# Kernel tuning notes

Hardware: AMD Instinct MI355X
Metric: run time of the kernel (lower is better)

## Reference

```python
import jax, jax.numpy as jnp
import numpy as np
import math

SQRT32 = math.sqrt(32.0)


def _l2norm(x, eps=1e-12):
    # matches torch.nn.functional.normalize(dim=-1): x / max(||x||, eps)
    n = jnp.linalg.norm(x, axis=-1, keepdims=True)
    return x / jnp.maximum(n, eps)


def setup_inputs() -> dict:
    key = jax.random.key(0)
    k1, k2 = jax.random.split(key)
    z = jax.random.normal(k1, (8, 256, 32, 32), dtype=jnp.float32)
    # trunc_normal_(std=0.02) init approximated by scaled normal
    embed_weight = jax.random.normal(k2, (16384, 256), dtype=jnp.float32) * 0.02
    return {"z": z, "embed_weight": embed_weight}


def reference(z, embed_weight):
    # z: [b, d, h, w] channel-first -> pack to [b*h*w, d]
    b, d, h, w = z.shape
    zf = jnp.transpose(z, (0, 2, 3, 1)).reshape(-1, d)  # [N, d]

    # l2_norm=True, no predefined codebook: distance = -z @ normalize(E)^T
    ew = _l2norm(embed_weight)                          # [K, d]
    dist = -(zf @ ew.T)                                 # [N, K]
    min_encoding_indices = jnp.argmin(dist, axis=1)     # [N]

    # gather UNnormalized embedding rows, then normalize (as in source)
    z_q = _l2norm(embed_weight[min_encoding_indices])   # [N, d]

    # straight-through estimator
    z_q = zf + jax.lax.stop_gradient(z_q - zf)

    loss = jnp.zeros((1,), dtype=z.dtype)

    # unpack to [b, h, w, d]
    zq_bhwd = z_q.reshape(b, h, w, d)
    # torch .long() truncates toward zero; astype(int) does the same
    bit_indices = (zq_bhwd * SQRT32).astype(jnp.int32) + 4
    zq_out = jnp.transpose(zq_bhwd, (0, 3, 1, 2))       # [b, d, h, w]

    return zq_out, min_encoding_indices, bit_indices, loss
```

## Files before the change

kernel.cpp:

```cpp
#include <hip/hip_runtime.h>
#include <math.h>

#define D      256
#define K      16384
#define NPTS   8192
#define DELTA  0.2f
#define LCAP   512
#define MAXCAP 4000000u

#define O_IDX  2097152
#define O_BIT  2105344
#define O_LOSS 4202496

typedef __attribute__((ext_vector_type(8))) short bf16x8;
typedef __attribute__((ext_vector_type(4))) float f32x4;
typedef unsigned long long u64;

__device__ __forceinline__ unsigned f2s(float f) {
    unsigned u = __float_as_uint(f);
    return (u & 0x80000000u) ? ~u : (u | 0x80000000u);
}
__device__ __forceinline__ float s2f(unsigned s) {
    return __uint_as_float((s & 0x80000000u) ? (s & 0x7fffffffu) : ~s);
}
__device__ __forceinline__ unsigned short f2bf(float f) {
    unsigned u = __float_as_uint(f);
    u += 0x7fffu + ((u >> 16) & 1u);
    return (unsigned short)(u >> 16);
}

__device__ __forceinline__ void gload16(const unsigned short* g, unsigned short* l) {
    __builtin_amdgcn_global_load_lds(
        (const __attribute__((address_space(1))) unsigned int*)g,
        (__attribute__((address_space(3))) unsigned int*)l, 16, 0, 0);
}


__global__ __launch_bounds__(256) void prep(const float* __restrict__ E,
                                            const float* __restrict__ z,
                                            float* __restrict__ den,
                                            unsigned short* __restrict__ ewbT,
                                            unsigned short* __restrict__ zfbT,
                                            float* __restrict__ zf32,
                                            unsigned* __restrict__ gmax,
                                            u64* __restrict__ keys,
                                            unsigned* __restrict__ cnt) {
    const int blk = blockIdx.x, tid = threadIdx.x;
    if (blk < 512) {
        const int lane = tid & 63, wave = tid >> 6;
        if (blk < 32)        gmax[blk * 256 + tid] = 0u;
        else if (blk < 64)   keys[(blk - 32) * 256 + tid] = 0ull;
        else if (blk == 64 && tid < 2) cnt[tid] = 0u;
        #pragma unroll
        for (int j = 0; j < 8; ++j) {
            const int row = blk * 32 + wave * 8 + j;
            const float4 v = *(const float4*)(E + (size_t)row * D + lane * 4);
            float ss = v.x * v.x + v.y * v.y + v.z * v.z + v.w * v.w;
            #pragma unroll
            for (int o = 1; o < 64; o <<= 1) ss += __shfl_xor(ss, o);
            const float dn = fmaxf(sqrtf(ss), 1e-12f);
            const unsigned lo = (unsigned)f2bf(v.x / dn) | ((unsigned)f2bf(v.y / dn) << 16);
            const unsigned hi = (unsigned)f2bf(v.z / dn) | ((unsigned)f2bf(v.w / dn) << 16);
            *(uint2*)(ewbT + ((size_t)(lane >> 1) * K + row) * 8 + (lane & 1) * 4)
                = make_uint2(lo, hi);
            if (lane == 0) den[row] = dn;
        }
    } else {
        const int bi = blk - 512;
        const int b = bi >> 4, hw0 = (bi & 15) * 64;
        __shared__ float t[64][65];
        for (int dc = 0; dc < D; dc += 64) {
            #pragma unroll
            for (int it = 0; it < 16; ++it) {
                const int idx = it * 256 + tid;
                const int dl = idx >> 6, hw = idx & 63;
                t[dl][hw] = z[(size_t)(b * 256 + dc + dl) * 1024 + hw0 + hw];
            }
            __syncthreads();
            #pragma unroll
            for (int it = 0; it < 16; ++it) {
                const int idx = it * 256 + tid;
                const int pl = idx >> 6, dl = idx & 63;
                const float v = t[dl][pl];
                const int p = b * 1024 + hw0 + pl, k = dc + dl;
                zfbT[((size_t)(k >> 3) * NPTS + p) * 8 + (k & 7)] = f2bf(v);
                zf32[(size_t)p * D + k] = v;
            }
            __syncthreads();
        }
    }
}


#define STAGE(buf, t)                                                               \
    do {                                                                            \
        const size_t oA_ = (size_t)(t) * (4 * NPTS * 8);                            \
        const size_t oB_ = (size_t)(t) * (4 * K * 8);                               \
        gload16(gA0_ + oA_, &sA[buf][tid * 8]);                                     \
        gload16(gA1_ + oA_, &sA[buf][2048 + tid * 8]);                              \
        gload16(gB0_ + oB_, &sB[buf][tid * 8]);                                     \
        gload16(gB1_ + oB_, &sB[buf][2048 + tid * 8]);                              \
    } while (0)

#define COMPUTE(buf)                                                                \
    do {                                                                            \
        bf16x8 af_[4], bf_[4];                                                      \
        const unsigned short* a_ = &sA[buf][(size_t)sbA_ * 8];                      \
        const unsigned short* b_ = &sB[buf][(size_t)sbB_ * 8];                      \
        _Pragma("unroll")                                                           \
        for (int mt = 0; mt < 4; ++mt) {                                            \
            af_[mt] = *(const bf16x8*)(a_ + mt * 128);                              \
            bf_[mt] = *(const bf16x8*)(b_ + mt * 128);                              \
        }                                                                           \
        __builtin_amdgcn_s_setprio(1);                                              \
        _Pragma("unroll")                                                           \
        for (int mt = 0; mt < 4; ++mt)                                              \
            _Pragma("unroll")                                                       \
            for (int nt = 0; nt < 4; ++nt)                                          \
                acc[mt][nt] = __builtin_amdgcn_mfma_f32_16x16x32_bf16(af_[mt], bf_[nt], \
                                                                      acc[mt][nt], 0, 0, 0); \
        __builtin_amdgcn_s_setprio(0);                                              \
    } while (0)

#define WAITBAR(VM)                                                                 \
    asm volatile("s_waitcnt vmcnt(" VM ")" ::: "memory");                           \
    __builtin_amdgcn_s_barrier();                                                   \
    asm volatile("" ::: "memory");

#define GEMM_CORE()                                                                 \
    __shared__ unsigned short sA[3][4096];                                          \
    __shared__ unsigned short sB[3][4096];                                          \
    f32x4 acc[4][4];                                                                \
    _Pragma("unroll")                                                               \
    for (int i_ = 0; i_ < 4; ++i_)                                                  \
        _Pragma("unroll")                                                           \
        for (int j_ = 0; j_ < 4; ++j_) acc[i_][j_] = (f32x4){0.f, 0.f, 0.f, 0.f};   \
    const int q0_ = tid >> 7, q1_ = q0_ + 2, pp_ = tid & 127;                       \
    const unsigned short* gA0_ = zfbT + ((size_t)q0_ * NPTS + m0 + (pp_ ^ (q0_ << 1))) * 8; \
    const unsigned short* gA1_ = zfbT + ((size_t)q1_ * NPTS + m0 + (pp_ ^ (q1_ << 1))) * 8; \
    const unsigned short* gB0_ = ewbT + ((size_t)q0_ * K + n0 + (pp_ ^ (q0_ << 1))) * 8; \
    const unsigned short* gB1_ = ewbT + ((size_t)q1_ * K + n0 + (pp_ ^ (q1_ << 1))) * 8; \
    const int sbA_ = quad * 128 + ((wm * 64 + col) ^ (quad << 1));                  \
    const int sbB_ = quad * 128 + ((wn * 64 + col) ^ (quad << 1));                  \
    STAGE(0, 0);                                                                    \
    STAGE(1, 1);                                                                    \
    WAITBAR("4") STAGE(2, 2); COMPUTE(0);                                           \
    WAITBAR("4") STAGE(0, 3); COMPUTE(1);                                           \
    WAITBAR("4") STAGE(1, 4); COMPUTE(2);                                           \
    WAITBAR("4") STAGE(2, 5); COMPUTE(0 + 0);                        \
    WAITBAR("4") STAGE(0, 6); COMPUTE(1);                            \
    WAITBAR("4") STAGE(1, 7); COMPUTE(2);                            \
    WAITBAR("4")              COMPUTE(0);                            \
    WAITBAR("0")              COMPUTE(1);

__global__ __launch_bounds__(256, 3) void score_seed(const unsigned short* __restrict__ zfbT,
                                                     const unsigned short* __restrict__ ewbT,
                                                     unsigned* __restrict__ gmax,
                                                     u64* __restrict__ cand,
                                                     unsigned* __restrict__ cnt,
                                                     unsigned cap) {
    __shared__ unsigned thrS[128];
    __shared__ u64 lbuf[LCAP];
    __shared__ unsigned lcount, lbase;

    const int tid = threadIdx.x, lane = tid & 63, wave = tid >> 6;
    const int quad = lane >> 4, col = lane & 15;
    const int wm = wave >> 1, wn = wave & 1;
    const int m0 = blockIdx.x * 128;
    const int n0 = blockIdx.y * 128;
    const int shsrc = lane & 48;

    if (tid < 128) thrS[tid] = 0u;
    if (tid == 0) lcount = 0u;

    GEMM_CORE()
    __syncthreads();

    float red[4][4];
    #pragma unroll
    for (int mt = 0; mt < 4; ++mt)
        #pragma unroll
        for (int r = 0; r < 4; ++r)
            red[mt][r] = fmaxf(fmaxf(acc[mt][0][r], acc[mt][1][r]),
                               fmaxf(acc[mt][2][r], acc[mt][3][r]));
    #pragma unroll
    for (int off = 1; off < 16; off <<= 1)
        #pragma unroll
        for (int mt = 0; mt < 4; ++mt)
            #pragma unroll
            for (int r = 0; r < 4; ++r)
                red[mt][r] = fmaxf(red[mt][r], __shfl_xor(red[mt][r], off));
    #pragma unroll
    for (int mt = 0; mt < 4; ++mt)
        #pragma unroll
        for (int r = 0; r < 4; ++r) {
            const int pl = wm * 64 + mt * 16 + quad * 4 + r;
            unsigned cur = 0;
            if (col == 0) {
                const unsigned enc = f2s(red[mt][r]);
                const unsigned old = atomicMax(&thrS[pl], enc);
                cur = old > enc ? old : enc;
            }
            cur = (unsigned)__shfl((int)cur, shsrc);
            red[mt][r] = s2f(cur) - DELTA;
        }

    const int ncode0 = n0 + wn * 64 + col;
    #pragma unroll
    for (int mt = 0; mt < 4; ++mt) {
        #pragma unroll
        for (int r = 0; r < 4; ++r) {
            const float tp = red[mt][r];
            const unsigned pt = m0 + wm * 64 + mt * 16 + quad * 4 + r;
            #pragma unroll
            for (int nt = 0; nt < 4; ++nt) {
                const float v = acc[mt][nt][r];
                if (v >= tp) {
                    const unsigned slot = atomicAdd(&lcount, 1u);
                    const u64 e = ((u64)((pt << 14) | (unsigned)(ncode0 + nt * 16)) << 32)
                                  | f2s(v);
                    if (slot < LCAP) lbuf[slot] = e;
                    else {
                        const unsigned g = atomicAdd(cnt, 1u);
                        if (g < cap) cand[g] = e;
                    }
                }
            }
        }
    }

    __syncthreads();
    if (tid < 128) atomicMax(&gmax[m0 + tid], thrS[tid]);
    const unsigned m_ = lcount < LCAP ? lcount : LCAP;
    if (tid == 0) lbase = atomicAdd(cnt, m_);
    __syncthreads();
    for (unsigned i = tid; i < m_; i += 256) {
        const unsigned g = lbase + i;
        if (g < cap) cand[g] = lbuf[i];
    }
}

__global__ __launch_bounds__(256, 3) void score_main(const unsigned short* __restrict__ zfbT,
                                                     const unsigned short* __restrict__ ewbT,
                                                     const unsigned* __restrict__ gmax,
                                                     u64* __restrict__ cand,
                                                     unsigned* __restrict__ cnt,
                                                     unsigned cap) {
    __shared__ float thrL[128];
    __shared__ u64 lbuf[LCAP];
    __shared__ unsigned lcount, lbase;

    const int tid = threadIdx.x, lane = tid & 63, wave = tid >> 6;
    const int quad = lane >> 4, col = lane & 15;
    const int wm = wave >> 1, wn = wave & 1;
    const int m0 = blockIdx.x * 128;
    const int n0 = (16 + blockIdx.y) * 128;

    if (tid < 128) thrL[tid] = s2f(gmax[m0 + tid]) - DELTA;
    if (tid == 0) lcount = 0u;

    GEMM_CORE()
    __syncthreads();

    const int ncode0 = n0 + wn * 64 + col;
    #pragma unroll
    for (int mt = 0; mt < 4; ++mt) {
        #pragma unroll
        for (int r = 0; r < 4; ++r) {
            const int pl = wm * 64 + mt * 16 + quad * 4 + r;
            const float tp = thrL[pl];
            #pragma unroll
            for (int nt = 0; nt < 4; ++nt) {
                const float v = acc[mt][nt][r];
                if (v >= tp) {
                    const unsigned slot = atomicAdd(&lcount, 1u);
                    const u64 e = ((u64)(((unsigned)pl + m0) << 14 | (unsigned)(ncode0 + nt * 16)) << 32)
                                  | f2s(v);
                    if (slot < LCAP) lbuf[slot] = e;
                    else {
                        const unsigned g = atomicAdd(cnt, 1u);
                        if (g < cap) cand[g] = e;
                    }
                }
            }
        }
    }

    __syncthreads();
    const unsigned m_ = lcount < LCAP ? lcount : LCAP;
    if (tid == 0) lbase = atomicAdd(cnt, m_);
    __syncthreads();
    for (unsigned i = tid; i < m_; i += 256) {
        const unsigned g = lbase + i;
        if (g < cap) cand[g] = lbuf[i];
    }
}

__global__ __launch_bounds__(256) void cand_max(const u64* __restrict__ cand,
                                                const unsigned* __restrict__ cnt,
                                                unsigned* __restrict__ gmax,
                                                unsigned cap) {
    const unsigned total = min(cnt[0], cap);
    const unsigned stride = gridDim.x * 256;
    for (unsigned i = blockIdx.x * 256 + threadIdx.x; i < total; i += stride) {
        const u64 e = cand[i];
        atomicMax(&gmax[(unsigned)(e >> 46)], (unsigned)(e & 0xffffffffull));
    }
}

__global__ __launch_bounds__(256) void rescore(const float* __restrict__ zf32,
                                               const float* __restrict__ E,
                                               const float* __restrict__ den,
                                               const unsigned* __restrict__ gmax,
                                               const u64* __restrict__ cand,
                                               const unsigned* __restrict__ cnt,
                                               u64* __restrict__ keys,
                                               unsigned cap) {
    const unsigned total = min(cnt[0], cap);
    const int lane = threadIdx.x & 63;
    const unsigned w = (blockIdx.x * 256 + threadIdx.x) >> 6;
    const unsigned nw = gridDim.x * 4;
    for (unsigned base = w * 64; base < total; base += nw * 64) {
        const unsigned i = base + lane;
        u64 e = 0;
        bool keep = false;
        if (i < total) {
            e = cand[i];
            const int p = (int)(e >> 46);
            keep = (s2f((unsigned)(e & 0xffffffffull)) >= s2f(gmax[p]) - DELTA);
        }
        u64 mask = __ballot(keep);
        while (mask) {
            const int src = __ffsll((long long)mask) - 1;
            mask &= mask - 1;
            const unsigned pc = (unsigned)__shfl((int)(unsigned)(e >> 32), src);
            const int p = pc >> 14, c = pc & 16383;
            const float dinv = 1.0f / den[c];
            const float4 a = *(const float4*)(zf32 + (size_t)p * D + lane * 4);
            const float4 b = *(const float4*)(E + (size_t)c * D + lane * 4);
            float sv = fmaf(a.x, b.x * dinv, fmaf(a.y, b.y * dinv,
                       fmaf(a.z, b.z * dinv, a.w * (b.w * dinv))));
            #pragma unroll
            for (int o = 1; o < 64; o <<= 1) sv += __shfl_xor(sv, o);
            if (lane == 0)
                atomicMax(keys + p, ((u64)f2s(sv) << 32) | (unsigned)(16383 - c));
        }
    }
}

__global__ __launch_bounds__(256) void finalize(const float* __restrict__ E,
                                                const float* __restrict__ den,
                                                const u64* __restrict__ keys,
                                                float* __restrict__ out) {
    __shared__ float t[32][257];
    __shared__ int sIdx[32];
    __shared__ float sDen[32];
    const int tid = threadIdx.x;
    const int n0 = blockIdx.x * 32;
    if (tid < 32) {
        const u64 key = keys[n0 + tid];
        const int idx = 16383 - (int)(unsigned)(key & 0xffffffffull);
        sIdx[tid] = idx;
        sDen[tid] = den[idx];
        out[O_IDX + n0 + tid] = (float)idx;
    }
    __syncthreads();
    const float S = 5.65685424949238019520675489683895f;
    #pragma unroll 4
    for (int i = 0; i < 32; ++i) {
        const float v = E[(size_t)sIdx[i] * D + tid] / sDen[i];
        t[i][tid] = v;
        out[O_BIT + (size_t)(n0 + i) * D + tid] = (float)((int)(v * S) + 4);
    }
    __syncthreads();
    const int b = n0 >> 10, hw0 = n0 & 1023;
    const int hwl = tid & 31, cg = tid >> 5;
    #pragma unroll 4
    for (int cc = 0; cc < 32; ++cc) {
        const int c = cc * 8 + cg;
        out[(size_t)(b * 256 + c) * 1024 + hw0 + hwl] = t[hwl][c];
    }
    if (n0 == 0 && tid == 0) out[O_LOSS] = 0.0f;
}

extern "C" void kernel_launch(void* const* d_in, const int* in_sizes, int n_in,
                              void* d_out, int out_size, void* d_ws, size_t ws_size,
                              hipStream_t stream) {
    const float* z = (const float*)d_in[0];
    const float* E = (const float*)d_in[1];
    float* out = (float*)d_out;

    char* w = (char*)d_ws;
    unsigned short* ewbT = (unsigned short*)w;  w += (size_t)K * D * 2;
    unsigned short* zfbT = (unsigned short*)w;  w += (size_t)NPTS * D * 2;
    float*          zf32 = (float*)w;           w += (size_t)NPTS * D * 4;
    u64*            keys = (u64*)w;             w += (size_t)NPTS * 8;
    float*          den  = (float*)w;           w += (size_t)K * 4;
    unsigned*       gmax = (unsigned*)w;        w += (size_t)NPTS * 4;
    unsigned*       cnt  = (unsigned*)w;        w += 256;
    u64*            cand = (u64*)w;
    const size_t fixed = (size_t)(w - (char*)d_ws);
    const size_t avail = ws_size > fixed ? (ws_size - fixed) / 8 : 0;
    const unsigned cap = (unsigned)(avail < (size_t)MAXCAP ? avail : (size_t)MAXCAP);

    prep<<<640, 256, 0, stream>>>(E, z, den, ewbT, zfbT, zf32, gmax, keys, cnt);

    dim3 gpre(NPTS / 128, 16);
    score_seed<<<gpre, 256, 0, stream>>>(zfbT, ewbT, gmax, cand, cnt, cap);
    dim3 gmain(NPTS / 128, 112);
    score_main<<<gmain, 256, 0, stream>>>(zfbT, ewbT, gmax, cand, cnt, cap);

    cand_max<<<256, 256, 0, stream>>>(cand, cnt, gmax, cap);
    rescore<<<1024, 256, 0, stream>>>(zf32, E, den, gmax, cand, cnt, keys, cap);
    finalize<<<NPTS / 32, 256, 0, stream>>>(E, den, keys, out);
}
```

Before: 260.9 us.

## Enlarge GEMM tiles to 256x256 with 512 threads, double-buffered K64 stages

```diff
diff --git a/kernel.cpp b/kernel.cpp
--- a/kernel.cpp
+++ b/kernel.cpp
@@ -5,7 +5,7 @@
 #define K      16384
 #define NPTS   8192
 #define DELTA  0.2f
-#define LCAP   512
+#define LCAP   2048
 #define MAXCAP 4000000u
 
 #define O_IDX  2097152
@@ -33,6 +33,10 @@
     __builtin_amdgcn_global_load_lds(
         (const __attribute__((address_space(1))) unsigned int*)g,
         (__attribute__((address_space(3))) unsigned int*)l, 16, 0, 0);
+}
+
+__device__ __forceinline__ unsigned lds_off(const void* p) {
+    return (unsigned)(size_t)(const __attribute__((address_space(3))) void*)p;
 }
 
 
@@ -94,27 +98,47 @@
 
 #define STAGE(buf, t)                                                               \
     do {                                                                            \
-        const size_t oA_ = (size_t)(t) * (4 * NPTS * 8);                            \
-        const size_t oB_ = (size_t)(t) * (4 * K * 8);                               \
-        gload16(gA0_ + oA_, &sA[buf][tid * 8]);                                     \
-        gload16(gA1_ + oA_, &sA[buf][2048 + tid * 8]);                              \
-        gload16(gB0_ + oB_, &sB[buf][tid * 8]);                                     \
-        gload16(gB1_ + oB_, &sB[buf][2048 + tid * 8]);                              \
+        const size_t oA_ = (size_t)(t) * (8u * NPTS * 8);                           \
+        const size_t oB_ = (size_t)(t) * (8u * K * 8);                              \
+        unsigned short* dA_ = &sA[buf][0][0][0];                                    \
+        unsigned short* dB_ = &sB[buf][0][0][0];                                    \
+        gload16(gA0_ + oA_, dA_ + (size_t)tid * 8);                                 \
+        gload16(gA1_ + oA_, dA_ + (size_t)(512 + tid) * 8);                         \
+        gload16(gA2_ + oA_, dA_ + (size_t)(1024 + tid) * 8);                        \
+        gload16(gA3_ + oA_, dA_ + (size_t)(1536 + tid) * 8);                        \
+        gload16(gB0_ + oB_, dB_ + (size_t)tid * 8);                                 \
+        gload16(gB1_ + oB_, dB_ + (size_t)(512 + tid) * 8);                         \
+        gload16(gB2_ + oB_, dB_ + (size_t)(1024 + tid) * 8);                        \
+        gload16(gB3_ + oB_, dB_ + (size_t)(1536 + tid) * 8);                        \
     } while (0)
 
-#define COMPUTE(buf)                                                                \
+#define RKK(buf, AA, BB)                                                            \
     do {                                                                            \
-        bf16x8 af_[4], bf_[4];                                                      \
-        const unsigned short* a_ = &sA[buf][(size_t)sbA_ * 8];                      \
-        const unsigned short* b_ = &sB[buf][(size_t)sbB_ * 8];                      \
-        _Pragma("unroll")                                                           \
-        for (int mt = 0; mt < 4; ++mt) {                                            \
-            af_[mt] = *(const bf16x8*)(a_ + mt * 128);                              \
-            bf_[mt] = *(const bf16x8*)(b_ + mt * 128);                              \
-        }                                                                           \
+        const unsigned a__ = (AA) + (unsigned)((buf) * 32768);                      \
+        const unsigned b__ = (BB) + (unsigned)((buf) * 32768);                      \
+        asm volatile("ds_read_b128 %0, %1"             : "=v"(af_[0]) : "v"(a__));  \
+        asm volatile("ds_read_b128 %0, %1 offset:256"  : "=v"(af_[1]) : "v"(a__));  \
+        asm volatile("ds_read_b128 %0, %1 offset:512"  : "=v"(af_[2]) : "v"(a__));  \
+        asm volatile("ds_read_b128 %0, %1 offset:768"  : "=v"(af_[3]) : "v"(a__));  \
+        asm volatile("ds_read_b128 %0, %1 offset:1024" : "=v"(af_[4]) : "v"(a__));  \
+        asm volatile("ds_read_b128 %0, %1 offset:1280" : "=v"(af_[5]) : "v"(a__));  \
+        asm volatile("ds_read_b128 %0, %1 offset:1536" : "=v"(af_[6]) : "v"(a__));  \
+        asm volatile("ds_read_b128 %0, %1 offset:1792" : "=v"(af_[7]) : "v"(a__));  \
+        asm volatile("ds_read_b128 %0, %1"             : "=v"(bf_[0]) : "v"(b__));  \
+        asm volatile("ds_read_b128 %0, %1 offset:256"  : "=v"(bf_[1]) : "v"(b__));  \
+        asm volatile("ds_read_b128 %0, %1 offset:512"  : "=v"(bf_[2]) : "v"(b__));  \
+        asm volatile("ds_read_b128 %0, %1 offset:768"  : "=v"(bf_[3]) : "v"(b__));  \
+    } while (0)
+
+#define LGKM_SB                                                                     \
+    asm volatile("s_waitcnt lgkmcnt(0)" ::: "memory");                              \
+    __builtin_amdgcn_sched_barrier(0);
+
+#define MFMAS                                                                       \
+    do {                                                                            \
         __builtin_amdgcn_s_setprio(1);                                              \
         _Pragma("unroll")                                                           \
-        for (int mt = 0; mt < 4; ++mt)                                              \
+        for (int mt = 0; mt < 8; ++mt)                                              \
             _Pragma("unroll")                                                       \
             for (int nt = 0; nt < 4; ++nt)                                          \
                 acc[mt][nt] = __builtin_amdgcn_mfma_f32_16x16x32_bf16(af_[mt], bf_[nt], \
@@ -127,58 +151,94 @@
     __builtin_amdgcn_s_barrier();                                                   \
     asm volatile("" ::: "memory");
 
+#define BARFENCE                                                                    \
+    __builtin_amdgcn_s_barrier();                                                   \
+    asm volatile("" ::: "memory");
+
 #define GEMM_CORE()                                                                 \
-    __shared__ unsigned short sA[3][4096];                                          \
-    __shared__ unsigned short sB[3][4096];                                          \
-    f32x4 acc[4][4];                                                                \
+    __shared__ unsigned short sA[2][8][256][8];                                     \
+    __shared__ unsigned short sB[2][8][256][8];                                     \
+    f32x4 acc[8][4];                                                                \
     _Pragma("unroll")                                                               \
-    for (int i_ = 0; i_ < 4; ++i_)                                                  \
+    for (int i_ = 0; i_ < 8; ++i_)                                                  \
         _Pragma("unroll")                                                           \
         for (int j_ = 0; j_ < 4; ++j_) acc[i_][j_] = (f32x4){0.f, 0.f, 0.f, 0.f};   \
-    const int q0_ = tid >> 7, q1_ = q0_ + 2, pp_ = tid & 127;                       \
-    const unsigned short* gA0_ = zfbT + ((size_t)q0_ * NPTS + m0 + (pp_ ^ (q0_ << 1))) * 8; \
-    const unsigned short* gA1_ = zfbT + ((size_t)q1_ * NPTS + m0 + (pp_ ^ (q1_ << 1))) * 8; \
-    const unsigned short* gB0_ = ewbT + ((size_t)q0_ * K + n0 + (pp_ ^ (q0_ << 1))) * 8; \
-    const unsigned short* gB1_ = ewbT + ((size_t)q1_ * K + n0 + (pp_ ^ (q1_ << 1))) * 8; \
-    const int sbA_ = quad * 128 + ((wm * 64 + col) ^ (quad << 1));                  \
-    const int sbB_ = quad * 128 + ((wn * 64 + col) ^ (quad << 1));                  \
+    bf16x8 af_[8], bf_[4];                                                          \
+    const int th_ = tid & 255, hi_ = tid >> 8;                                      \
+    const int c0_ = hi_, c1_ = 2 + hi_, c2_ = 4 + hi_, c3_ = 6 + hi_;               \
+    const unsigned short* gA0_ = zfbT + ((size_t)c0_ * NPTS + m0 + (th_ ^ (c0_ << 1))) * 8; \
+    const unsigned short* gA1_ = zfbT + ((size_t)c1_ * NPTS + m0 + (th_ ^ (c1_ << 1))) * 8; \
+    const unsigned short* gA2_ = zfbT + ((size_t)c2_ * NPTS + m0 + (th_ ^ (c2_ << 1))) * 8; \
+    const unsigned short* gA3_ = zfbT + ((size_t)c3_ * NPTS + m0 + (th_ ^ (c3_ << 1))) * 8; \
+    const unsigned short* gB0_ = ewbT + ((size_t)c0_ * K + n0 + (th_ ^ (c0_ << 1))) * 8; \
+    const unsigned short* gB1_ = ewbT + ((size_t)c1_ * K + n0 + (th_ ^ (c1_ << 1))) * 8; \
+    const unsigned short* gB2_ = ewbT + ((size_t)c2_ * K + n0 + (th_ ^ (c2_ << 1))) * 8; \
+    const unsigned short* gB3_ = ewbT + ((size_t)c3_ * K + n0 + (th_ ^ (c3_ << 1))) * 8; \
+    const unsigned sAb_ = lds_off(&sA[0][0][0][0]);                                 \
+    const unsigned sBb_ = lds_off(&sB[0][0][0][0]);                                 \
+    const int ck0_ = quad, ck1_ = 4 + quad;                                         \
+    const unsigned aA0_ = sAb_ + (unsigned)((ck0_ * 256 + ((wm * 128 + col) ^ (ck0_ << 1))) * 16); \
+    const unsigned aA1_ = sAb_ + (unsigned)((ck1_ * 256 + ((wm * 128 + col) ^ (ck1_ << 1))) * 16); \
+    const unsigned bB0_ = sBb_ + (unsigned)((ck0_ * 256 + ((wn * 64 + col) ^ (ck0_ << 1))) * 16); \
+    const unsigned bB1_ = sBb_ + (unsigned)((ck1_ * 256 + ((wn * 64 + col) ^ (ck1_ << 1))) * 16); \
     STAGE(0, 0);                                                                    \
     STAGE(1, 1);                                                                    \
-    WAITBAR("4") STAGE(2, 2); COMPUTE(0);                                           \
-    WAITBAR("4") STAGE(0, 3); COMPUTE(1);                                           \
-    WAITBAR("4") STAGE(1, 4); COMPUTE(2);                                           \
-    WAITBAR("4") STAGE(2, 5); COMPUTE(0 + 0);                        \
-    WAITBAR("4") STAGE(0, 6); COMPUTE(1);                            \
-    WAITBAR("4") STAGE(1, 7); COMPUTE(2);                            \
-    WAITBAR("4")              COMPUTE(0);                            \
-    WAITBAR("0")              COMPUTE(1);
-
-__global__ __launch_bounds__(256, 3) void score_seed(const unsigned short* __restrict__ zfbT,
+    WAITBAR("8")                                                                    \
+    RKK(0, aA0_, bB0_); LGKM_SB; MFMAS;                                             \
+    RKK(0, aA1_, bB1_); LGKM_SB; BARFENCE; STAGE(0, 2); MFMAS;                      \
+    WAITBAR("8")                                                                    \
+    RKK(1, aA0_, bB0_); LGKM_SB; MFMAS;                                             \
+    RKK(1, aA1_, bB1_); LGKM_SB; BARFENCE; STAGE(1, 3); MFMAS;                      \
+    WAITBAR("8")                                                                    \
+    RKK(0, aA0_, bB0_); LGKM_SB; MFMAS;                                             \
+    RKK(0, aA1_, bB1_); LGKM_SB; MFMAS;                                             \
+    WAITBAR("0")                                                                    \
+    RKK(1, aA0_, bB0_); LGKM_SB; MFMAS;                                             \
+    RKK(1, aA1_, bB1_); LGKM_SB; MFMAS;
+
+#define CAND_APPEND(e)                                                              \
+    do {                                                                            \
+        const u64 am_ = __builtin_amdgcn_read_exec();                               \
+        const unsigned n_ = (unsigned)__popcll(am_);                                \
+        const unsigned rk_ = (unsigned)__popcll(am_ & ((1ull << lane) - 1));        \
+        unsigned base_ = 0;                                                         \
+        if (rk_ == 0) base_ = atomicAdd(cnt, n_);                                   \
+        base_ = (unsigned)__builtin_amdgcn_readfirstlane((int)base_);               \
+        const unsigned g_ = base_ + rk_;                                            \
+        if (g_ < cap) cand[g_] = (e);                                               \
+    } while (0)
+
+#define XCD_DECODE(NT0)                                                             \
+    const unsigned bid_ = blockIdx.x;                                               \
+    const unsigned j_ = bid_ >> 3;                                                  \
+    const int m0 = (int)(((bid_ & 7u) << 2) | (j_ & 3u)) * 256;                     \
+    const int n0 = (NT0) + (int)(j_ >> 2) * 256;
+
+__global__ __launch_bounds__(512, 2) void score_seed(const unsigned short* __restrict__ zfbT,
                                                      const unsigned short* __restrict__ ewbT,
                                                      unsigned* __restrict__ gmax,
                                                      u64* __restrict__ cand,
                                                      unsigned* __restrict__ cnt,
                                                      unsigned cap) {
-    __shared__ unsigned thrS[128];
+    __shared__ unsigned thrS[256];
     __shared__ u64 lbuf[LCAP];
     __shared__ unsigned lcount, lbase;
 
     const int tid = threadIdx.x, lane = tid & 63, wave = tid >> 6;
     const int quad = lane >> 4, col = lane & 15;
-    const int wm = wave >> 1, wn = wave & 1;
-    const int m0 = blockIdx.x * 128;
-    const int n0 = blockIdx.y * 128;
+    const int wm = wave >> 2, wn = wave & 3;
+    XCD_DECODE(0)
     const int shsrc = lane & 48;
 
-    if (tid < 128) thrS[tid] = 0u;
+    if (tid < 256) thrS[tid] = 0u;
     if (tid == 0) lcount = 0u;
 
     GEMM_CORE()
     __syncthreads();
 
-    float red[4][4];
+    float red[8][4];
     #pragma unroll
-    for (int mt = 0; mt < 4; ++mt)
+    for (int mt = 0; mt < 8; ++mt)
         #pragma unroll
         for (int r = 0; r < 4; ++r)
             red[mt][r] = fmaxf(fmaxf(acc[mt][0][r], acc[mt][1][r]),
@@ -186,15 +246,15 @@
     #pragma unroll
     for (int off = 1; off < 16; off <<= 1)
         #pragma unroll
-        for (int mt = 0; mt < 4; ++mt)
+        for (int mt = 0; mt < 8; ++mt)
             #pragma unroll
             for (int r = 0; r < 4; ++r)
                 red[mt][r] = fmaxf(red[mt][r], __shfl_xor(red[mt][r], off));
     #pragma unroll
-    for (int mt = 0; mt < 4; ++mt)
+    for (int mt = 0; mt < 8; ++mt)
         #pragma unroll
         for (int r = 0; r < 4; ++r) {
-            const int pl = wm * 64 + mt * 16 + quad * 4 + r;
+            const int pl = wm * 128 + mt * 16 + quad * 4 + r;
             unsigned cur = 0;
             if (col == 0) {
                 const unsigned enc = f2s(red[mt][r]);
@@ -207,11 +267,11 @@
 
     const int ncode0 = n0 + wn * 64 + col;
     #pragma unroll
-    for (int mt = 0; mt < 4; ++mt) {
+    for (int mt = 0; mt < 8; ++mt) {
         #pragma unroll
         for (int r = 0; r < 4; ++r) {
             const float tp = red[mt][r];
-            const unsigned pt = m0 + wm * 64 + mt * 16 + quad * 4 + r;
+            const unsigned pt = m0 + wm * 128 + mt * 16 + quad * 4 + r;
             #pragma unroll
             for (int nt = 0; nt < 4; ++nt) {
                 const float v = acc[mt][nt][r];
@@ -220,43 +280,39 @@
                     const u64 e = ((u64)((pt << 14) | (unsigned)(ncode0 + nt * 16)) << 32)
                                   | f2s(v);
                     if (slot < LCAP) lbuf[slot] = e;
-                    else {
-                        const unsigned g = atomicAdd(cnt, 1u);
-                        if (g < cap) cand[g] = e;
-                    }
+                    else CAND_APPEND(e);
                 }
             }
         }
     }
 
     __syncthreads();
-    if (tid < 128) atomicMax(&gmax[m0 + tid], thrS[tid]);
+    if (tid < 256) atomicMax(&gmax[m0 + tid], thrS[tid]);
     const unsigned m_ = lcount < LCAP ? lcount : LCAP;
     if (tid == 0) lbase = atomicAdd(cnt, m_);
     __syncthreads();
-    for (unsigned i = tid; i < m_; i += 256) {
+    for (unsigned i = tid; i < m_; i += 512) {
         const unsigned g = lbase + i;
         if (g < cap) cand[g] = lbuf[i];
     }
 }
 
-__global__ __launch_bounds__(256, 3) void score_main(const unsigned short* __restrict__ zfbT,
+__global__ __launch_bounds__(512, 2) void score_main(const unsigned short* __restrict__ zfbT,
                                                      const unsigned short* __restrict__ ewbT,
                                                      const unsigned* __restrict__ gmax,
                                                      u64* __restrict__ cand,
                                                      unsigned* __restrict__ cnt,
                                                      unsigned cap) {
-    __shared__ float thrL[128];
+    __shared__ float thrL[256];
     __shared__ u64 lbuf[LCAP];
     __shared__ unsigned lcount, lbase;
 
     const int tid = threadIdx.x, lane = tid & 63, wave = tid >> 6;
     const int quad = lane >> 4, col = lane & 15;
-    const int wm = wave >> 1, wn = wave & 1;
-    const int m0 = blockIdx.x * 128;
-    const int n0 = (16 + blockIdx.y) * 128;
-
-    if (tid < 128) thrL[tid] = s2f(gmax[m0 + tid]) - DELTA;
+    const int wm = wave >> 2, wn = wave & 3;
+    XCD_DECODE(2048)
+
+    if (tid < 256) thrL[tid] = s2f(gmax[m0 + tid]) - DELTA;
     if (tid == 0) lcount = 0u;
 
     GEMM_CORE()
@@ -264,10 +320,10 @@
 
     const int ncode0 = n0 + wn * 64 + col;
     #pragma unroll
-    for (int mt = 0; mt < 4; ++mt) {
+    for (int mt = 0; mt < 8; ++mt) {
         #pragma unroll
         for (int r = 0; r < 4; ++r) {
-            const int pl = wm * 64 + mt * 16 + quad * 4 + r;
+            const int pl = wm * 128 + mt * 16 + quad * 4 + r;
             const float tp = thrL[pl];
             #pragma unroll
             for (int nt = 0; nt < 4; ++nt) {
@@ -277,10 +333,7 @@
                     const u64 e = ((u64)(((unsigned)pl + m0) << 14 | (unsigned)(ncode0 + nt * 16)) << 32)
                                   | f2s(v);
                     if (slot < LCAP) lbuf[slot] = e;
-                    else {
-                        const unsigned g = atomicAdd(cnt, 1u);
-                        if (g < cap) cand[g] = e;
-                    }
+                    else CAND_APPEND(e);
                 }
             }
         }
@@ -290,7 +343,7 @@
     const unsigned m_ = lcount < LCAP ? lcount : LCAP;
     if (tid == 0) lbase = atomicAdd(cnt, m_);
     __syncthreads();
-    for (unsigned i = tid; i < m_; i += 256) {
+    for (unsigned i = tid; i < m_; i += 512) {
         const unsigned g = lbase + i;
         if (g < cap) cand[g] = lbuf[i];
     }
@@ -405,10 +458,8 @@
 
     prep<<<640, 256, 0, stream>>>(E, z, den, ewbT, zfbT, zf32, gmax, keys, cnt);
 
-    dim3 gpre(NPTS / 128, 16);
-    score_seed<<<gpre, 256, 0, stream>>>(zfbT, ewbT, gmax, cand, cnt, cap);
-    dim3 gmain(NPTS / 128, 112);
-    score_main<<<gmain, 256, 0, stream>>>(zfbT, ewbT, gmax, cand, cnt, cap);
+    score_seed<<<256, 512, 0, stream>>>(zfbT, ewbT, gmax, cand, cnt, cap);
+    score_main<<<1792, 512, 0, stream>>>(zfbT, ewbT, gmax, cand, cnt, cap);
 
     cand_max<<<256, 256, 0, stream>>>(cand, cnt, gmax, cap);
     rescore<<<1024, 256, 0, stream>>>(zf32, E, den, gmax, cand, cnt, keys, cap);
```

Result: faster. 234.5 us (-10.1%).
